# Kernel tuning notes

Measured on AMD Instinct MI355X. Metric: run time of the kernel, lower is better.

Reference implementation:

```python
import jax, jax.numpy as jnp
import numpy as np

B, N, K, D, H = 4, 8192, 16, 128, 4
DK = D // H  # key_dim = num_hiddens // num_heads
NEG_INF = -1e9


def setup_inputs() -> dict:
    key = jax.random.key(0)
    ks = jax.random.split(key, 16)
    s = 1.0 / np.sqrt(D)
    return {
        "vertex_feat": jax.random.normal(ks[0], (B, N, D), dtype=jnp.float32),
        "neighbors_idx": jax.random.randint(ks[1], (B, N, K), 0, N, dtype=jnp.int32),
        "valid_lens": jax.random.randint(ks[2], (B, N), 0, K, dtype=jnp.int32),
        # MultiHeadAttention projections (keras EinsumDense with bias)
        "Wq": (jax.random.normal(ks[3], (D, H, DK)) * s).astype(jnp.float32),
        "bq": jnp.zeros((H, DK), jnp.float32),
        "Wk": (jax.random.normal(ks[4], (D, H, DK)) * s).astype(jnp.float32),
        "bk": jnp.zeros((H, DK), jnp.float32),
        "Wv": (jax.random.normal(ks[5], (D, H, DK)) * s).astype(jnp.float32),
        "bv": jnp.zeros((H, DK), jnp.float32),
        "Wo": (jax.random.normal(ks[6], (H, DK, D)) * s).astype(jnp.float32),
        "bo": jnp.zeros((D,), jnp.float32),
        # MLP: Dense(D, relu) -> Dense(D)
        "W1": (jax.random.normal(ks[7], (D, D)) * s).astype(jnp.float32),
        "b1": jnp.zeros((D,), jnp.float32),
        "W2": (jax.random.normal(ks[8], (D, D)) * s).astype(jnp.float32),
        "b2": jnp.zeros((D,), jnp.float32),
    }


def reference(vertex_feat, neighbors_idx, valid_lens,
              Wq, bq, Wk, bk, Wv, bv, Wo, bo, W1, b1, W2, b2):
    # query: [B, N, 1, D]; gathered neighbors (batch_dims=1): [B, N, K, D]
    q = vertex_feat[:, :, None, :]
    neigh = jax.vmap(lambda vf, idx: vf[idx])(vertex_feat, neighbors_idx)
    value = jnp.concatenate([q, neigh], axis=2)  # [B, N, K+1, D]

    # per-head projections
    qh = jnp.einsum('bnqd,dhk->bnqhk', q, Wq) + bq      # [B,N,1,H,DK]
    kh = jnp.einsum('bnsd,dhk->bnshk', value, Wk) + bk  # [B,N,K+1,H,DK]
    vh = jnp.einsum('bnsd,dhk->bnshk', value, Wv) + bv

    # attention over the neighbor axis (attention_axes=(2,))
    scores = jnp.einsum('bnqhk,bnshk->bnhqs', qh, kh) / np.sqrt(DK)  # [B,N,H,1,K+1]
    # mask: positions < valid_lens + 1 (self + valid neighbors)
    pos = jnp.arange(K + 1)[None, None, :]                # [1,1,K+1]
    mask = pos < (valid_lens + 1)[:, :, None]             # [B,N,K+1] bool
    scores = scores + jnp.where(mask, 0.0, NEG_INF)[:, :, None, None, :]
    attn = jax.nn.softmax(scores, axis=-1)                # [B,N,H,1,K+1]

    ctx = jnp.einsum('bnhqs,bnshk->bnqhk', attn, vh)      # [B,N,1,H,DK]
    out = jnp.einsum('bnqhk,hkd->bnqd', ctx, Wo) + bo     # [B,N,1,D]
    out = out[:, :, 0, :]                                  # squeeze -> [B,N,D]

    # MLP (dropout inactive at inference)
    h = jax.nn.relu(out @ W1 + b1)
    new_vertex_feat = h @ W2 + b2
    return new_vertex_feat
```

## Files before the change

kernel.cpp:

```cpp
#include <hip/hip_runtime.h>
#include <math.h>

#define BB 4
#define NN 8192
#define KNB 16
#define DD 128
#define SS 17
#define M_TOT (BB*NN)

typedef __attribute__((ext_vector_type(8))) short          bf8;
typedef __attribute__((ext_vector_type(4))) float          f4;
typedef __attribute__((ext_vector_type(4))) unsigned short u16x4;

static __device__ __forceinline__ unsigned short f2bf(float f) {
    unsigned u = __builtin_bit_cast(unsigned, f);
    u += 0x7fffu + ((u >> 16) & 1u);
    return (unsigned short)(u >> 16);
}
static __device__ __forceinline__ float bf2f(unsigned short h) {
    return __builtin_bit_cast(float, (unsigned)h << 16);
}

__global__ __launch_bounds__(256) void cvt_x(const float* __restrict__ in,
                                             unsigned short* __restrict__ out)
{
    int i = blockIdx.x * 256 + threadIdx.x;
    float4 v = ((const float4*)in)[i];
    u16x4 r;
    r[0] = f2bf(v.x); r[1] = f2bf(v.y); r[2] = f2bf(v.z); r[3] = f2bf(v.w);
    *((u16x4*)out + i) = r;
}

__global__ __launch_bounds__(256) void cvt_wT(
    const float* __restrict__ Wq, const float* __restrict__ Wk,
    const float* __restrict__ Wv, const float* __restrict__ Wo,
    const float* __restrict__ W1, const float* __restrict__ W2,
    unsigned short* __restrict__ out)
{
    int m = blockIdx.x >> 4;
    const float* src = (m == 0) ? Wq : (m == 1) ? Wk : (m == 2) ? Wv
                     : (m == 3) ? Wo : (m == 4) ? W1 : W2;
    unsigned short* dst = out + m * 16384;
    int o = (blockIdx.x & 15) * 1024 + threadIdx.x * 4;
    int n = o >> 7, k = o & 127;
    u16x4 r;
    #pragma unroll
    for (int i = 0; i < 4; ++i) r[i] = f2bf(src[(size_t)(k + i) * 128 + n]);
    *(u16x4*)(dst + o) = r;
}

__global__ __launch_bounds__(256) void gemm_mfma(
    const unsigned short* __restrict__ X, const unsigned short* __restrict__ Wt,
    const float* __restrict__ bias, unsigned short* __restrict__ Yb,
    float* __restrict__ Yf, int relu, int f32out)
{
    __shared__ unsigned short Ws[128 * 136];

    const int tid = threadIdx.x;

    #pragma unroll
    for (int i = 0; i < 8; ++i) {
        int c = tid + i * 256;
        int n = c >> 4, k8 = c & 15;
        bf8 val = ((const bf8*)Wt)[c];
        *(bf8*)(Ws + n * 136 + k8 * 8) = val;
    }

    const int lane = tid & 63;
    const int wv   = tid >> 6;
    const int wm   = wv >> 1;
    const int wn   = wv & 1;
    const int ln   = lane & 15;
    const int quad = lane >> 4;
    const int row0 = blockIdx.x * 64 + wm * 32;

    __syncthreads();

    bf8 bfr[4][4];
    #pragma unroll
    for (int t = 0; t < 4; ++t)
        #pragma unroll
        for (int s = 0; s < 4; ++s)
            bfr[t][s] = *(const bf8*)(Ws + (wn * 64 + t * 16 + ln) * 136 + s * 32 + quad * 8);

    f4 acc[2][4] = {};

    #pragma unroll
    for (int s = 0; s < 4; ++s) {
        bf8 a0 = *(const bf8*)(X + (size_t)(row0 + ln)      * DD + s * 32 + quad * 8);
        bf8 a1 = *(const bf8*)(X + (size_t)(row0 + 16 + ln) * DD + s * 32 + quad * 8);
        #pragma unroll
        for (int t = 0; t < 4; ++t) {
            acc[0][t] = __builtin_amdgcn_mfma_f32_16x16x32_bf16(a0, bfr[t][s], acc[0][t], 0, 0, 0);
            acc[1][t] = __builtin_amdgcn_mfma_f32_16x16x32_bf16(a1, bfr[t][s], acc[1][t], 0, 0, 0);
        }
    }

    #pragma unroll
    for (int mt = 0; mt < 2; ++mt) {
        #pragma unroll
        for (int t = 0; t < 4; ++t) {
            const int col  = wn * 64 + t * 16 + ln;
            const float bc = bias[col];
            #pragma unroll
            for (int r = 0; r < 4; ++r) {
                const int row = row0 + mt * 16 + quad * 4 + r;
                float v = acc[mt][t][r] + bc;
                if (relu) v = fmaxf(v, 0.f);
                if (f32out) Yf[(size_t)row * DD + col] = v;
                else        Yb[(size_t)row * DD + col] = f2bf(v);
            }
        }
    }
}

__global__ __launch_bounds__(256) void attn_kernel(
    const unsigned short* __restrict__ Qh, const unsigned short* __restrict__ Kh,
    const unsigned short* __restrict__ Vh, const int* __restrict__ nbr,
    const int* __restrict__ vlen, unsigned short* __restrict__ Ctx)
{
    const int lane = threadIdx.x & 63;
    const int wv   = threadIdx.x >> 6;
    const int pair = lane >> 5;
    const int c    = lane & 31;
    const int v    = blockIdx.x * 8 + wv * 2 + pair;
    const int b    = v >> 13;

    const u16x4 qu = ((const u16x4*)Qh)[(size_t)v * 32 + c];
    const float q0 = bf2f(qu[0]), q1 = bf2f(qu[1]), q2 = bf2f(qu[2]), q3 = bf2f(qu[3]);

    int rows[SS];
    rows[0] = v;
    #pragma unroll
    for (int s = 1; s < SS; ++s)
        rows[s] = b * NN + nbr[(size_t)v * KNB + (s - 1)];

    float sc[SS];
    #pragma unroll
    for (int s = 0; s < SS; ++s) {
        u16x4 ku = ((const u16x4*)Kh)[(size_t)rows[s] * 32 + c];
        float p = q0 * bf2f(ku[0]) + q1 * bf2f(ku[1]) + q2 * bf2f(ku[2]) + q3 * bf2f(ku[3]);
        p += __shfl_xor(p, 1, 8);
        p += __shfl_xor(p, 2, 8);
        p += __shfl_xor(p, 4, 8);
        sc[s] = p * 0.17677669529663687f;
    }

    const int len = vlen[v];
    float m = sc[0];
    #pragma unroll
    for (int s = 1; s < SS; ++s) m = (s <= len) ? fmaxf(m, sc[s]) : m;
    float sum = 0.f;
    #pragma unroll
    for (int s = 0; s < SS; ++s) {
        float e = (s <= len) ? __expf(sc[s] - m) : 0.f;
        sc[s] = e;
        sum += e;
    }
    const float inv = 1.f / sum;

    float a0 = 0.f, a1 = 0.f, a2 = 0.f, a3 = 0.f;
    #pragma unroll
    for (int s = 0; s < SS; ++s) {
        u16x4 vu = ((const u16x4*)Vh)[(size_t)rows[s] * 32 + c];
        float w = sc[s] * inv;
        a0 = fmaf(w, bf2f(vu[0]), a0);
        a1 = fmaf(w, bf2f(vu[1]), a1);
        a2 = fmaf(w, bf2f(vu[2]), a2);
        a3 = fmaf(w, bf2f(vu[3]), a3);
    }
    u16x4 r;
    r[0] = f2bf(a0); r[1] = f2bf(a1); r[2] = f2bf(a2); r[3] = f2bf(a3);
    ((u16x4*)Ctx)[(size_t)v * 32 + c] = r;
}

extern "C" void kernel_launch(void* const* d_in, const int* in_sizes, int n_in,
                              void* d_out, int out_size, void* d_ws, size_t ws_size,
                              hipStream_t stream)
{
    const float* vf   = (const float*)d_in[0];
    const int*   nbr  = (const int*)  d_in[1];
    const int*   vlen = (const int*)  d_in[2];
    const float* Wq   = (const float*)d_in[3];
    const float* bq   = (const float*)d_in[4];
    const float* Wk   = (const float*)d_in[5];
    const float* bk   = (const float*)d_in[6];
    const float* Wv   = (const float*)d_in[7];
    const float* bv   = (const float*)d_in[8];
    const float* Wo   = (const float*)d_in[9];
    const float* bo   = (const float*)d_in[10];
    const float* W1   = (const float*)d_in[11];
    const float* b1   = (const float*)d_in[12];
    const float* W2   = (const float*)d_in[13];
    const float* b2   = (const float*)d_in[14];

    float* out = (float*)d_out;

    const size_t SZ = (size_t)M_TOT * DD;
    unsigned short* Xb   = (unsigned short*)d_ws;
    unsigned short* WtT  = Xb + SZ;
    unsigned short* qh   = WtT + 6 * 16384;
    unsigned short* kh   = qh + SZ;
    unsigned short* vh   = kh + SZ;
    unsigned short* ctx  = vh + SZ;
    unsigned short* obuf = ctx + SZ;
    unsigned short* hbuf = obuf + SZ;

    unsigned short* WqT = WtT;
    unsigned short* WkT = WtT + 16384;
    unsigned short* WvT = WtT + 2 * 16384;
    unsigned short* WoT = WtT + 3 * 16384;
    unsigned short* W1T = WtT + 4 * 16384;
    unsigned short* W2T = WtT + 5 * 16384;

    cvt_x <<<SZ / 1024, 256, 0, stream>>>(vf, Xb);
    cvt_wT<<<96,        256, 0, stream>>>(Wq, Wk, Wv, Wo, W1, W2, WtT);

    const int gg = M_TOT / 64;

    gemm_mfma<<<gg, 256, 0, stream>>>(Xb, WqT, bq, qh, nullptr, 0, 0);
    gemm_mfma<<<gg, 256, 0, stream>>>(Xb, WkT, bk, kh, nullptr, 0, 0);
    gemm_mfma<<<gg, 256, 0, stream>>>(Xb, WvT, bv, vh, nullptr, 0, 0);

    attn_kernel<<<M_TOT / 8, 256, 0, stream>>>(qh, kh, vh, nbr, vlen, ctx);

    gemm_mfma<<<gg, 256, 0, stream>>>(ctx,  WoT, bo, obuf, nullptr, 0, 0);
    gemm_mfma<<<gg, 256, 0, stream>>>(obuf, W1T, b1, hbuf, nullptr, 1, 0);
    gemm_mfma<<<gg, 256, 0, stream>>>(hbuf, W2T, b2, nullptr, out,  0, 1);
}
```

Baseline: 163.9 us.

## Fuse QKV projections and fuse attention with output projection and MLP

Replaces the separate input conversion and three QKV GEMM launches with one kernel. That kernel converts a 64-row tile of fp32 input to bf16 in LDS and runs all three projections from it, reloading each weight into shared memory in turn. The attention step is merged with the Wo, W1 and W2 GEMMs: each block computes context for 64 rows into LDS and chains the three GEMMs there, writing only the final fp32 output. This removes the global round trips for the bf16 input, context and intermediate activations, plus several launches. In exchange, attention now runs 8 vertices per 32-lane group serially with fewer blocks, which may hide gather latency less well.

```diff
diff --git a/kernel.cpp b/kernel.cpp
--- a/kernel.cpp
+++ b/kernel.cpp
@@ -7,6 +7,7 @@
 #define DD 128
 #define SS 17
 #define M_TOT (BB*NN)
+#define WPAD 136
 
 typedef __attribute__((ext_vector_type(8))) short          bf8;
 typedef __attribute__((ext_vector_type(4))) float          f4;
@@ -19,16 +20,6 @@
 }
 static __device__ __forceinline__ float bf2f(unsigned short h) {
     return __builtin_bit_cast(float, (unsigned)h << 16);
-}
-
-__global__ __launch_bounds__(256) void cvt_x(const float* __restrict__ in,
-                                             unsigned short* __restrict__ out)
-{
-    int i = blockIdx.x * 256 + threadIdx.x;
-    float4 v = ((const float4*)in)[i];
-    u16x4 r;
-    r[0] = f2bf(v.x); r[1] = f2bf(v.y); r[2] = f2bf(v.z); r[3] = f2bf(v.w);
-    *((u16x4*)out + i) = r;
 }
 
 __global__ __launch_bounds__(256) void cvt_wT(
@@ -49,129 +40,242 @@
     *(u16x4*)(dst + o) = r;
 }
 
-__global__ __launch_bounds__(256) void gemm_mfma(
-    const unsigned short* __restrict__ X, const unsigned short* __restrict__ Wt,
-    const float* __restrict__ bias, unsigned short* __restrict__ Yb,
-    float* __restrict__ Yf, int relu, int f32out)
+__global__ __launch_bounds__(256) void qkv_kernel(
+    const float* __restrict__ X, const unsigned short* __restrict__ WtT,
+    const float* __restrict__ bq, const float* __restrict__ bk,
+    const float* __restrict__ bv,
+    unsigned short* __restrict__ qh, unsigned short* __restrict__ kh,
+    unsigned short* __restrict__ vh)
 {
-    __shared__ unsigned short Ws[128 * 136];
-
-    const int tid = threadIdx.x;
-
+    __shared__ unsigned short Xs[64 * WPAD];
+    __shared__ unsigned short Wb[128 * WPAD];
+
+    const int tid  = threadIdx.x;
+    const int row0 = blockIdx.x * 64;
+
+    {
+        const float4* Xg = (const float4*)(X + (size_t)row0 * DD);
+        #pragma unroll
+        for (int i = 0; i < 8; ++i) {
+            int idx = tid + i * 256;
+            int r = idx >> 5, c4 = idx & 31;
+            float4 v = Xg[idx];
+            u16x4 u;
+            u[0] = f2bf(v.x); u[1] = f2bf(v.y); u[2] = f2bf(v.z); u[3] = f2bf(v.w);
+            *(u16x4*)(Xs + r * WPAD + c4 * 4) = u;
+        }
+    }
     #pragma unroll
     for (int i = 0; i < 8; ++i) {
         int c = tid + i * 256;
         int n = c >> 4, k8 = c & 15;
-        bf8 val = ((const bf8*)Wt)[c];
-        *(bf8*)(Ws + n * 136 + k8 * 8) = val;
-    }
-
-    const int lane = tid & 63;
-    const int wv   = tid >> 6;
-    const int wm   = wv >> 1;
-    const int wn   = wv & 1;
-    const int ln   = lane & 15;
-    const int quad = lane >> 4;
-    const int row0 = blockIdx.x * 64 + wm * 32;
-
+        *(bf8*)(Wb + n * WPAD + k8 * 8) = ((const bf8*)WtT)[c];
+    }
+
+    const int lane = tid & 63, wv = tid >> 6;
+    const int wm = wv >> 1, wn = wv & 1;
+    const int ln = lane & 15, quad = lane >> 4;
     __syncthreads();
 
-    bf8 bfr[4][4];
-    #pragma unroll
-    for (int t = 0; t < 4; ++t)
+    bf8 afr[2][4];
+    #pragma unroll
+    for (int mt = 0; mt < 2; ++mt)
         #pragma unroll
         for (int s = 0; s < 4; ++s)
-            bfr[t][s] = *(const bf8*)(Ws + (wn * 64 + t * 16 + ln) * 136 + s * 32 + quad * 8);
-
-    f4 acc[2][4] = {};
-
-    #pragma unroll
-    for (int s = 0; s < 4; ++s) {
-        bf8 a0 = *(const bf8*)(X + (size_t)(row0 + ln)      * DD + s * 32 + quad * 8);
-        bf8 a1 = *(const bf8*)(X + (size_t)(row0 + 16 + ln) * DD + s * 32 + quad * 8);
-        #pragma unroll
-        for (int t = 0; t < 4; ++t) {
-            acc[0][t] = __builtin_amdgcn_mfma_f32_16x16x32_bf16(a0, bfr[t][s], acc[0][t], 0, 0, 0);
-            acc[1][t] = __builtin_amdgcn_mfma_f32_16x16x32_bf16(a1, bfr[t][s], acc[1][t], 0, 0, 0);
+            afr[mt][s] = *(const bf8*)(Xs + (wm * 32 + mt * 16 + ln) * WPAD + s * 32 + quad * 8);
+
+    const float* biases[3] = { bq, bk, bv };
+    unsigned short* outs[3] = { qh, kh, vh };
+
+    #pragma unroll
+    for (int g = 0; g < 3; ++g) {
+        bf8 bfr[4][4];
+        #pragma unroll
+        for (int t = 0; t < 4; ++t)
+            #pragma unroll
+            for (int s = 0; s < 4; ++s)
+                bfr[t][s] = *(const bf8*)(Wb + (wn * 64 + t * 16 + ln) * WPAD + s * 32 + quad * 8);
+        __syncthreads();
+
+        if (g < 2) {
+            const bf8* Wn = (const bf8*)(WtT + (g + 1) * 16384);
+            #pragma unroll
+            for (int i = 0; i < 8; ++i) {
+                int c = tid + i * 256;
+                int n = c >> 4, k8 = c & 15;
+                *(bf8*)(Wb + n * WPAD + k8 * 8) = Wn[c];
+            }
         }
-    }
-
-    #pragma unroll
-    for (int mt = 0; mt < 2; ++mt) {
-        #pragma unroll
-        for (int t = 0; t < 4; ++t) {
-            const int col  = wn * 64 + t * 16 + ln;
-            const float bc = bias[col];
-            #pragma unroll
-            for (int r = 0; r < 4; ++r) {
-                const int row = row0 + mt * 16 + quad * 4 + r;
-                float v = acc[mt][t][r] + bc;
-                if (relu) v = fmaxf(v, 0.f);
-                if (f32out) Yf[(size_t)row * DD + col] = v;
-                else        Yb[(size_t)row * DD + col] = f2bf(v);
-            }
-        }
-    }
-}
-
-__global__ __launch_bounds__(256) void attn_kernel(
+
+        f4 acc[2][4] = {};
+        #pragma unroll
+        for (int s = 0; s < 4; ++s)
+            #pragma unroll
+            for (int t = 0; t < 4; ++t) {
+                acc[0][t] = __builtin_amdgcn_mfma_f32_16x16x32_bf16(afr[0][s], bfr[t][s], acc[0][t], 0, 0, 0);
+                acc[1][t] = __builtin_amdgcn_mfma_f32_16x16x32_bf16(afr[1][s], bfr[t][s], acc[1][t], 0, 0, 0);
+            }
+
+        const float* bias = biases[g];
+        unsigned short* Y = outs[g];
+        #pragma unroll
+        for (int mt = 0; mt < 2; ++mt)
+            #pragma unroll
+            for (int t = 0; t < 4; ++t) {
+                int col = wn * 64 + t * 16 + ln;
+                float bc = bias[col];
+                #pragma unroll
+                for (int r = 0; r < 4; ++r) {
+                    int row = row0 + wm * 32 + mt * 16 + quad * 4 + r;
+                    Y[(size_t)row * DD + col] = f2bf(acc[mt][t][r] + bc);
+                }
+            }
+        __syncthreads();
+    }
+}
+
+__global__ __launch_bounds__(256) void attn_ffn_kernel(
     const unsigned short* __restrict__ Qh, const unsigned short* __restrict__ Kh,
     const unsigned short* __restrict__ Vh, const int* __restrict__ nbr,
-    const int* __restrict__ vlen, unsigned short* __restrict__ Ctx)
+    const int* __restrict__ vlen, const unsigned short* __restrict__ WtT3,
+    const float* __restrict__ bo, const float* __restrict__ b1,
+    const float* __restrict__ b2, float* __restrict__ Out)
 {
-    const int lane = threadIdx.x & 63;
-    const int wv   = threadIdx.x >> 6;
-    const int pair = lane >> 5;
-    const int c    = lane & 31;
-    const int v    = blockIdx.x * 8 + wv * 2 + pair;
-    const int b    = v >> 13;
-
-    const u16x4 qu = ((const u16x4*)Qh)[(size_t)v * 32 + c];
-    const float q0 = bf2f(qu[0]), q1 = bf2f(qu[1]), q2 = bf2f(qu[2]), q3 = bf2f(qu[3]);
-
-    int rows[SS];
-    rows[0] = v;
-    #pragma unroll
-    for (int s = 1; s < SS; ++s)
-        rows[s] = b * NN + nbr[(size_t)v * KNB + (s - 1)];
-
-    float sc[SS];
-    #pragma unroll
-    for (int s = 0; s < SS; ++s) {
-        u16x4 ku = ((const u16x4*)Kh)[(size_t)rows[s] * 32 + c];
-        float p = q0 * bf2f(ku[0]) + q1 * bf2f(ku[1]) + q2 * bf2f(ku[2]) + q3 * bf2f(ku[3]);
-        p += __shfl_xor(p, 1, 8);
-        p += __shfl_xor(p, 2, 8);
-        p += __shfl_xor(p, 4, 8);
-        sc[s] = p * 0.17677669529663687f;
-    }
-
-    const int len = vlen[v];
-    float m = sc[0];
-    #pragma unroll
-    for (int s = 1; s < SS; ++s) m = (s <= len) ? fmaxf(m, sc[s]) : m;
-    float sum = 0.f;
-    #pragma unroll
-    for (int s = 0; s < SS; ++s) {
-        float e = (s <= len) ? __expf(sc[s] - m) : 0.f;
-        sc[s] = e;
-        sum += e;
-    }
-    const float inv = 1.f / sum;
-
-    float a0 = 0.f, a1 = 0.f, a2 = 0.f, a3 = 0.f;
-    #pragma unroll
-    for (int s = 0; s < SS; ++s) {
-        u16x4 vu = ((const u16x4*)Vh)[(size_t)rows[s] * 32 + c];
-        float w = sc[s] * inv;
-        a0 = fmaf(w, bf2f(vu[0]), a0);
-        a1 = fmaf(w, bf2f(vu[1]), a1);
-        a2 = fmaf(w, bf2f(vu[2]), a2);
-        a3 = fmaf(w, bf2f(vu[3]), a3);
-    }
-    u16x4 r;
-    r[0] = f2bf(a0); r[1] = f2bf(a1); r[2] = f2bf(a2); r[3] = f2bf(a3);
-    ((u16x4*)Ctx)[(size_t)v * 32 + c] = r;
+    __shared__ unsigned short Ct[64 * WPAD];
+    __shared__ unsigned short Wb[128 * WPAD];
+
+    const int tid  = threadIdx.x;
+    const int row0 = blockIdx.x * 64;
+
+    #pragma unroll
+    for (int i = 0; i < 8; ++i) {
+        int c = tid + i * 256;
+        int n = c >> 4, k8 = c & 15;
+        *(bf8*)(Wb + n * WPAD + k8 * 8) = ((const bf8*)WtT3)[c];
+    }
+
+    {
+        const int grp = tid >> 5;
+        const int c   = tid & 31;
+        #pragma unroll 1
+        for (int it = 0; it < 8; ++it) {
+            const int vl = grp * 8 + it;
+            const int v  = row0 + vl;
+            const int b  = v >> 13;
+
+            u16x4 qu = ((const u16x4*)Qh)[(size_t)v * 32 + c];
+            const float q0 = bf2f(qu[0]), q1 = bf2f(qu[1]),
+                        q2 = bf2f(qu[2]), q3 = bf2f(qu[3]);
+
+            int rows[SS];
+            rows[0] = v;
+            #pragma unroll
+            for (int s = 1; s < SS; ++s)
+                rows[s] = b * NN + nbr[(size_t)v * KNB + (s - 1)];
+
+            float sc[SS];
+            #pragma unroll
+            for (int s = 0; s < SS; ++s) {
+                u16x4 ku = ((const u16x4*)Kh)[(size_t)rows[s] * 32 + c];
+                float p = q0 * bf2f(ku[0]) + q1 * bf2f(ku[1])
+                        + q2 * bf2f(ku[2]) + q3 * bf2f(ku[3]);
+                p += __shfl_xor(p, 1, 8);
+                p += __shfl_xor(p, 2, 8);
+                p += __shfl_xor(p, 4, 8);
+                sc[s] = p * 0.17677669529663687f;
+            }
+
+            const int len = vlen[v];
+            float m = sc[0];
+            #pragma unroll
+            for (int s = 1; s < SS; ++s) m = (s <= len) ? fmaxf(m, sc[s]) : m;
+            float sum = 0.f;
+            #pragma unroll
+            for (int s = 0; s < SS; ++s) {
+                float e = (s <= len) ? __expf(sc[s] - m) : 0.f;
+                sc[s] = e;
+                sum += e;
+            }
+            const float inv = 1.f / sum;
+
+            float a0 = 0.f, a1 = 0.f, a2 = 0.f, a3 = 0.f;
+            #pragma unroll
+            for (int s = 0; s < SS; ++s) {
+                u16x4 vu = ((const u16x4*)Vh)[(size_t)rows[s] * 32 + c];
+                float w = sc[s] * inv;
+                a0 = fmaf(w, bf2f(vu[0]), a0);
+                a1 = fmaf(w, bf2f(vu[1]), a1);
+                a2 = fmaf(w, bf2f(vu[2]), a2);
+                a3 = fmaf(w, bf2f(vu[3]), a3);
+            }
+            u16x4 r;
+            r[0] = f2bf(a0); r[1] = f2bf(a1); r[2] = f2bf(a2); r[3] = f2bf(a3);
+            *(u16x4*)(Ct + vl * WPAD + c * 4) = r;
+        }
+    }
+    __syncthreads();
+
+    const int lane = tid & 63, wvv = tid >> 6;
+    const int wm = wvv >> 1, wn = wvv & 1;
+    const int ln = lane & 15, quad = lane >> 4;
+
+    const float* biases[3] = { bo, b1, b2 };
+
+    #pragma unroll
+    for (int g = 0; g < 3; ++g) {
+        bf8 afr[2][4], bfr[4][4];
+        #pragma unroll
+        for (int mt = 0; mt < 2; ++mt)
+            #pragma unroll
+            for (int s = 0; s < 4; ++s)
+                afr[mt][s] = *(const bf8*)(Ct + (wm * 32 + mt * 16 + ln) * WPAD + s * 32 + quad * 8);
+        #pragma unroll
+        for (int t = 0; t < 4; ++t)
+            #pragma unroll
+            for (int s = 0; s < 4; ++s)
+                bfr[t][s] = *(const bf8*)(Wb + (wn * 64 + t * 16 + ln) * WPAD + s * 32 + quad * 8);
+        __syncthreads();
+
+        if (g < 2) {
+            const bf8* Wn = (const bf8*)(WtT3 + (g + 1) * 16384);
+            #pragma unroll
+            for (int i = 0; i < 8; ++i) {
+                int c = tid + i * 256;
+                int n = c >> 4, k8 = c & 15;
+                *(bf8*)(Wb + n * WPAD + k8 * 8) = Wn[c];
+            }
+        }
+
+        f4 acc[2][4] = {};
+        #pragma unroll
+        for (int s = 0; s < 4; ++s)
+            #pragma unroll
+            for (int t = 0; t < 4; ++t) {
+                acc[0][t] = __builtin_amdgcn_mfma_f32_16x16x32_bf16(afr[0][s], bfr[t][s], acc[0][t], 0, 0, 0);
+                acc[1][t] = __builtin_amdgcn_mfma_f32_16x16x32_bf16(afr[1][s], bfr[t][s], acc[1][t], 0, 0, 0);
+            }
+
+        const float* bias = biases[g];
+        #pragma unroll
+        for (int mt = 0; mt < 2; ++mt)
+            #pragma unroll
+            for (int t = 0; t < 4; ++t) {
+                int col = wn * 64 + t * 16 + ln;
+                float bc = bias[col];
+                #pragma unroll
+                for (int r = 0; r < 4; ++r) {
+                    int rloc = wm * 32 + mt * 16 + quad * 4 + r;
+                    float vv = acc[mt][t][r] + bc;
+                    if (g == 2) {
+                        Out[(size_t)(row0 + rloc) * DD + col] = vv;
+                    } else {
+                        if (g == 1) vv = fmaxf(vv, 0.f);
+                        Ct[rloc * WPAD + col] = f2bf(vv);
+                    }
+                }
+            }
+        __syncthreads();
+    }
 }
 
 extern "C" void kernel_launch(void* const* d_in, const int* in_sizes, int n_in,
@@ -197,34 +301,15 @@
     float* out = (float*)d_out;
 
     const size_t SZ = (size_t)M_TOT * DD;
-    unsigned short* Xb   = (unsigned short*)d_ws;
-    unsigned short* WtT  = Xb + SZ;
-    unsigned short* qh   = WtT + 6 * 16384;
-    unsigned short* kh   = qh + SZ;
-    unsigned short* vh   = kh + SZ;
-    unsigned short* ctx  = vh + SZ;
-    unsigned short* obuf = ctx + SZ;
-    unsigned short* hbuf = obuf + SZ;
-
-    unsigned short* WqT = WtT;
-    unsigned short* WkT = WtT + 16384;
-    unsigned short* WvT = WtT + 2 * 16384;
-    unsigned short* WoT = WtT + 3 * 16384;
-    unsigned short* W1T = WtT + 4 * 16384;
-    unsigned short* W2T = WtT + 5 * 16384;
-
-    cvt_x <<<SZ / 1024, 256, 0, stream>>>(vf, Xb);
-    cvt_wT<<<96,        256, 0, stream>>>(Wq, Wk, Wv, Wo, W1, W2, WtT);
-
-    const int gg = M_TOT / 64;
-
-    gemm_mfma<<<gg, 256, 0, stream>>>(Xb, WqT, bq, qh, nullptr, 0, 0);
-    gemm_mfma<<<gg, 256, 0, stream>>>(Xb, WkT, bk, kh, nullptr, 0, 0);
-    gemm_mfma<<<gg, 256, 0, stream>>>(Xb, WvT, bv, vh, nullptr, 0, 0);
-
-    attn_kernel<<<M_TOT / 8, 256, 0, stream>>>(qh, kh, vh, nbr, vlen, ctx);
-
-    gemm_mfma<<<gg, 256, 0, stream>>>(ctx,  WoT, bo, obuf, nullptr, 0, 0);
-    gemm_mfma<<<gg, 256, 0, stream>>>(obuf, W1T, b1, hbuf, nullptr, 1, 0);
-    gemm_mfma<<<gg, 256, 0, stream>>>(hbuf, W2T, b2, nullptr, out,  0, 1);
-}
+    unsigned short* WtT = (unsigned short*)d_ws;
+    unsigned short* qh  = WtT + 6 * 16384;
+    unsigned short* kh  = qh + SZ;
+    unsigned short* vh  = kh + SZ;
+
+    cvt_wT<<<96, 256, 0, stream>>>(Wq, Wk, Wv, Wo, W1, W2, WtT);
+
+    qkv_kernel<<<M_TOT / 64, 256, 0, stream>>>(vf, WtT, bq, bk, bv, qh, kh, vh);
+
+    attn_ffn_kernel<<<M_TOT / 64, 256, 0, stream>>>(
+        qh, kh, vh, nbr, vlen, WtT + 3 * 16384, bo, b1, b2, out);
+}
```

After: 181.4 us. 1.11x slower.
